# Performance work log

Hardware: AMD Instinct MI355X
Metric: run time of the kernel (lower is better)

Reference implementation:

```python
import jax, jax.numpy as jnp
import numpy as np

TEMPERATURE = 8.0  # sqrt(d_head=64)
CLAMP = 15.0
EPS = 1e-6


def setup_inputs() -> dict:
    key = jax.random.key(0)
    kq, kk, kv, km = jax.random.split(key, 4)
    B, Lq, Lk, D = 16, 2048, 2048, 64
    q = jax.random.normal(kq, (B, Lq, D), dtype=jnp.float32)
    k = jax.random.normal(kk, (B, Lk, D), dtype=jnp.float32)
    v = jax.random.normal(kv, (B, Lk, D), dtype=jnp.float32)
    mask = jax.random.randint(km, (B, Lq, Lk), 0, 2).astype(jnp.float32)
    return {"q": q, "k": k, "v": v, "mask": mask}


def masked_softmax(x, m, axis=-1):
    # clamp -> multiply by mask -> stable exp -> multiply by mask -> normalize
    x = jnp.clip(x, -CLAMP, CLAMP)
    x = x * m
    e_x = jnp.exp(x - jnp.max(x, axis=axis, keepdims=True))
    e_x = e_x * m
    return e_x / (jnp.sum(e_x, axis=axis, keepdims=True) + EPS)


def reference(q, k, v, mask):
    # scores: [B, Lq, Lk]
    attn = jnp.einsum('bqd,bkd->bqk', q, k) / TEMPERATURE
    attn = masked_softmax(attn, mask, axis=2)
    # dropout is identity in eval mode (deterministic reference)
    output = jnp.einsum('bqk,bkd->bqd', attn, v)
    return (output, attn)
```

## Files before the change

### kernel.cpp

```cpp
#include <hip/hip_runtime.h>
#include <stdint.h>

#define NB 16
#define LQ 2048
#define LK 2048
#define DH 64
#define QT 32

typedef short bf16x8 __attribute__((ext_vector_type(8)));
typedef float f32x4 __attribute__((ext_vector_type(4)));

__device__ __forceinline__ unsigned short f2bf(float f) {
    union { float f; uint32_t u; } v; v.f = f;
    uint32_t u = v.u;
    u += 0x7FFFu + ((u >> 16) & 1u);
    return (unsigned short)(u >> 16);
}
__device__ __forceinline__ float bf2f(unsigned short h) {
    union { uint32_t u; float f; } v; v.u = ((uint32_t)h) << 16;
    return v.f;
}
__device__ __forceinline__ uint32_t pack2(float lo, float hi) {
    return (uint32_t)f2bf(lo) | ((uint32_t)f2bf(hi) << 16);
}

__global__ void convert_kernel(const float* __restrict__ q, const float* __restrict__ k,
                               const float* __restrict__ v,
                               unsigned short* __restrict__ qb,
                               unsigned short* __restrict__ kb,
                               unsigned short* __restrict__ vtb) {
    int bid = blockIdx.x;
    int tid = threadIdx.x;
    if (bid < 2048) {
        const float* src = (bid < 1024) ? q : k;
        unsigned short* dst = (bid < 1024) ? qb : kb;
        int64_t off = (int64_t)(bid & 1023) * 2048 + (int64_t)tid * 8;
        float4 a = *(const float4*)(src + off);
        float4 b4 = *(const float4*)(src + off + 4);
        uint4 o;
        o.x = pack2(a.x, a.y);
        o.y = pack2(a.z, a.w);
        o.z = pack2(b4.x, b4.y);
        o.w = pack2(b4.z, b4.w);
        *(uint4*)(dst + off) = o;
    } else {
        __shared__ unsigned short tile[64][72];
        int bid2 = bid - 2048;
        int bb = bid2 >> 5, kt = bid2 & 31;
        int k0 = kt * 64;
        int krow = tid >> 2, dc = (tid & 3) * 16;
        const float* vp = v + ((int64_t)(bb * LK) + k0 + krow) * DH + dc;
        float4 x0 = *(const float4*)(vp);
        float4 x1 = *(const float4*)(vp + 4);
        float4 x2 = *(const float4*)(vp + 8);
        float4 x3 = *(const float4*)(vp + 12);
        float vals[16] = {x0.x, x0.y, x0.z, x0.w, x1.x, x1.y, x1.z, x1.w,
                          x2.x, x2.y, x2.z, x2.w, x3.x, x3.y, x3.z, x3.w};
        #pragma unroll
        for (int i = 0; i < 16; ++i) tile[dc + i][krow] = f2bf(vals[i]);
        __syncthreads();
        int d = tid >> 2, kc = (tid & 3) * 16;
        uint4 r0 = *(const uint4*)&tile[d][kc];
        uint4 r1 = *(const uint4*)&tile[d][kc + 8];
        unsigned short* op = vtb + ((int64_t)(bb * DH) + d) * LK + k0 + kc;
        *(uint4*)op = r0;
        *(uint4*)(op + 8) = r1;
    }
}

__launch_bounds__(512, 1)
__global__ void attn_kernel(const unsigned short* __restrict__ qb,
                            const unsigned short* __restrict__ kb,
                            const unsigned short* __restrict__ vtb,
                            const float* __restrict__ mask,
                            float* __restrict__ out, float* __restrict__ attn) {
    extern __shared__ char smem[];
    float* denom_part = (float*)(smem + QT * LK * 2);

    int bid = blockIdx.x;
    int swz = (bid & 7) * 128 + (bid >> 3);
    int b = swz >> 6;
    int q0 = (swz & 63) * QT;

    int tid = threadIdx.x;
    int lane = tid & 63;
    int wave = tid >> 6;
    int wm = wave >> 2, wn = wave & 3;
    int lr = lane & 15, lg = lane >> 4;

    bf16x8 qf0, qf1;
    {
        const unsigned short* qp = qb + ((int64_t)(b * LQ + q0 + wm * 16 + lr)) * DH + 8 * lg;
        qf0 = *(const bf16x8*)qp;
        qf1 = *(const bf16x8*)(qp + 32);
    }

    float dsum[4] = {0.f, 0.f, 0.f, 0.f};

    for (int kt = 0; kt < LK / 64; ++kt) {
        int kbase = kt * 64 + wn * 16;
        const unsigned short* kp = kb + ((int64_t)(b * LK + kbase + lr)) * DH + 8 * lg;
        bf16x8 kf0 = *(const bf16x8*)kp;
        bf16x8 kf1 = *(const bf16x8*)(kp + 32);
        f32x4 acc = {0.f, 0.f, 0.f, 0.f};
        acc = __builtin_amdgcn_mfma_f32_16x16x32_bf16(qf0, kf0, acc, 0, 0, 0);
        acc = __builtin_amdgcn_mfma_f32_16x16x32_bf16(qf1, kf1, acc, 0, 0, 0);
        int c = kbase + lr;
        const float* mp = mask + ((int64_t)(b * LQ + q0 + wm * 16 + lg * 4)) * LK + c;
        #pragma unroll
        for (int j = 0; j < 4; ++j) {
            int r = wm * 16 + lg * 4 + j;
            float s = acc[j] * 0.125f;
            s = fminf(fmaxf(s, -15.0f), 15.0f);
            float m = mp[(int64_t)j * LK];
            float e = __expf(s * m) * m;
            unsigned short eb = f2bf(e);
            dsum[j] += bf2f(eb);
            int byteoff = (r * 4096 + c * 2) ^ ((r & 7) << 4);
            *(unsigned short*)(smem + byteoff) = eb;
        }
    }

    #pragma unroll
    for (int j = 0; j < 4; ++j) {
        float s = dsum[j];
        s += __shfl_xor(s, 1);
        s += __shfl_xor(s, 2);
        s += __shfl_xor(s, 4);
        s += __shfl_xor(s, 8);
        if (lr == 0) denom_part[wn * 32 + wm * 16 + lg * 4 + j] = s;
    }
    __syncthreads();

    f32x4 pacc = {0.f, 0.f, 0.f, 0.f};
    {
        const unsigned short* vp = vtb + ((int64_t)(b * DH + wn * 16 + lr)) * LK + 8 * lg;
        int r = wm * 16 + lr;
        int rowoff = r * 4096;
        int sw = (r & 7) << 4;
        for (int kk = 0; kk < LK; kk += 32) {
            int byteoff = (rowoff + (kk + 8 * lg) * 2) ^ sw;
            bf16x8 ef = *(const bf16x8*)(smem + byteoff);
            bf16x8 vf = *(const bf16x8*)(vp + kk);
            pacc = __builtin_amdgcn_mfma_f32_16x16x32_bf16(ef, vf, pacc, 0, 0, 0);
        }
    }

    #pragma unroll
    for (int j = 0; j < 4; ++j) {
        int r = wm * 16 + lg * 4 + j;
        float den = denom_part[r] + denom_part[32 + r] + denom_part[64 + r] +
                    denom_part[96 + r] + 1e-6f;
        out[((int64_t)(b * LQ + q0 + r)) * DH + wn * 16 + lr] = pacc[j] / den;
    }

    {
        int r = tid >> 4;
        float den = denom_part[r] + denom_part[32 + r] + denom_part[64 + r] +
                    denom_part[96 + r] + 1e-6f;
        float inv = 1.0f / den;
        float* ap = attn + ((int64_t)(b * LQ + q0 + r)) * LK;
        int rowoff = r * 4096;
        int sw = (r & 7) << 4;
        for (int c0 = (tid & 15) * 8; c0 < LK; c0 += 128) {
            int byteoff = (rowoff + c0 * 2) ^ sw;
            bf16x8 ev = *(const bf16x8*)(smem + byteoff);
            float4 o0, o1;
            o0.x = bf2f((unsigned short)ev[0]) * inv;
            o0.y = bf2f((unsigned short)ev[1]) * inv;
            o0.z = bf2f((unsigned short)ev[2]) * inv;
            o0.w = bf2f((unsigned short)ev[3]) * inv;
            o1.x = bf2f((unsigned short)ev[4]) * inv;
            o1.y = bf2f((unsigned short)ev[5]) * inv;
            o1.z = bf2f((unsigned short)ev[6]) * inv;
            o1.w = bf2f((unsigned short)ev[7]) * inv;
            *(float4*)(ap + c0) = o0;
            *(float4*)(ap + c0 + 4) = o1;
        }
    }
}

extern "C" void kernel_launch(void* const* d_in, const int* in_sizes, int n_in,
                              void* d_out, int out_size, void* d_ws, size_t ws_size,
                              hipStream_t stream) {
    const float* q    = (const float*)d_in[0];
    const float* k    = (const float*)d_in[1];
    const float* v    = (const float*)d_in[2];
    const float* mask = (const float*)d_in[3];
    float* out  = (float*)d_out;
    float* attn = out + (int64_t)NB * LQ * DH;

    unsigned short* qb  = (unsigned short*)d_ws;
    unsigned short* kb  = qb + (int64_t)NB * LQ * DH;
    unsigned short* vtb = kb + (int64_t)NB * LK * DH;

    (void)hipFuncSetAttribute((const void*)attn_kernel,
                              hipFuncAttributeMaxDynamicSharedMemorySize, 131584);

    convert_kernel<<<2560, 256, 0, stream>>>(q, k, v, qb, kb, vtb);
    attn_kernel<<<1024, 512, 131584, stream>>>(qb, kb, vtb, mask, out, attn);
}
```

Measured before the change: 257.6 us.

## Halve query tile, prefetch K/mask next tile, split PV reduction across waves

Reduces the query tile from 32 to 16 rows so each block uses about 68KB of LDS instead of 128KB, doubling the grid and letting more blocks co-reside per CU. All 8 waves now share the same 16 query rows and split the key dimension, with software prefetch of the next K fragment and mask values to hide global latency. The PV product is split into two key halves whose partial sums are combined through shared memory before normalization. Q is reloaded per smaller tile and an extra sync is added, in exchange for better latency hiding on the mask-bound score phase.

```diff
diff --git a/kernel.cpp b/kernel.cpp
--- a/kernel.cpp
+++ b/kernel.cpp
@@ -5,7 +5,7 @@
 #define LQ 2048
 #define LK 2048
 #define DH 64
-#define QT 32
+#define QT 16
 
 typedef short bf16x8 __attribute__((ext_vector_type(8)));
 typedef float f32x4 __attribute__((ext_vector_type(4)));
@@ -68,7 +68,7 @@
     }
 }
 
-__launch_bounds__(512, 1)
+__launch_bounds__(512, 4)
 __global__ void attn_kernel(const unsigned short* __restrict__ qb,
                             const unsigned short* __restrict__ kb,
                             const unsigned short* __restrict__ vtb,
@@ -76,48 +76,70 @@
                             float* __restrict__ out, float* __restrict__ attn) {
     extern __shared__ char smem[];
     float* denom_part = (float*)(smem + QT * LK * 2);
+    float* pp         = (float*)(smem + QT * LK * 2 + 512);
 
     int bid = blockIdx.x;
-    int swz = (bid & 7) * 128 + (bid >> 3);
-    int b = swz >> 6;
-    int q0 = (swz & 63) * QT;
+    int swz = (bid & 7) * 256 + (bid >> 3);
+    int b = swz >> 7;
+    int q0 = (swz & 127) * QT;
 
     int tid = threadIdx.x;
     int lane = tid & 63;
     int wave = tid >> 6;
-    int wm = wave >> 2, wn = wave & 3;
     int lr = lane & 15, lg = lane >> 4;
 
     bf16x8 qf0, qf1;
     {
-        const unsigned short* qp = qb + ((int64_t)(b * LQ + q0 + wm * 16 + lr)) * DH + 8 * lg;
+        const unsigned short* qp = qb + ((int64_t)(b * LQ + q0 + lr)) * DH + 8 * lg;
         qf0 = *(const bf16x8*)qp;
         qf1 = *(const bf16x8*)(qp + 32);
     }
 
     float dsum[4] = {0.f, 0.f, 0.f, 0.f};
 
-    for (int kt = 0; kt < LK / 64; ++kt) {
-        int kbase = kt * 64 + wn * 16;
-        const unsigned short* kp = kb + ((int64_t)(b * LK + kbase + lr)) * DH + 8 * lg;
-        bf16x8 kf0 = *(const bf16x8*)kp;
-        bf16x8 kf1 = *(const bf16x8*)(kp + 32);
-        f32x4 acc = {0.f, 0.f, 0.f, 0.f};
-        acc = __builtin_amdgcn_mfma_f32_16x16x32_bf16(qf0, kf0, acc, 0, 0, 0);
-        acc = __builtin_amdgcn_mfma_f32_16x16x32_bf16(qf1, kf1, acc, 0, 0, 0);
-        int c = kbase + lr;
-        const float* mp = mask + ((int64_t)(b * LQ + q0 + wm * 16 + lg * 4)) * LK + c;
-        #pragma unroll
-        for (int j = 0; j < 4; ++j) {
-            int r = wm * 16 + lg * 4 + j;
-            float s = acc[j] * 0.125f;
-            s = fminf(fmaxf(s, -15.0f), 15.0f);
-            float m = mp[(int64_t)j * LK];
-            float e = __expf(s * m) * m;
-            unsigned short eb = f2bf(e);
-            dsum[j] += bf2f(eb);
-            int byteoff = (r * 4096 + c * 2) ^ ((r & 7) << 4);
-            *(unsigned short*)(smem + byteoff) = eb;
+    {
+        const int64_t krow0 = (int64_t)b * LK;
+        const float* mbase = mask + ((int64_t)(b * LQ + q0 + lg * 4)) * LK;
+        bf16x8 kf0, kf1;
+        float mr0, mr1, mr2, mr3;
+        {
+            const unsigned short* kp =
+                kb + (krow0 + wave * 16 + lr) * DH + 8 * lg;
+            kf0 = *(const bf16x8*)kp;
+            kf1 = *(const bf16x8*)(kp + 32);
+            const float* mp = mbase + wave * 16 + lr;
+            mr0 = mp[0]; mr1 = mp[LK]; mr2 = mp[2 * LK]; mr3 = mp[3 * LK];
+        }
+        for (int kt = 0; kt < LK / 128; ++kt) {
+            bf16x8 nk0, nk1;
+            float nm0, nm1, nm2, nm3;
+            if (kt < LK / 128 - 1) {
+                int nbase = (kt + 1) * 128 + wave * 16;
+                const unsigned short* kp = kb + (krow0 + nbase + lr) * DH + 8 * lg;
+                nk0 = *(const bf16x8*)kp;
+                nk1 = *(const bf16x8*)(kp + 32);
+                const float* mp = mbase + nbase + lr;
+                nm0 = mp[0]; nm1 = mp[LK]; nm2 = mp[2 * LK]; nm3 = mp[3 * LK];
+            }
+            f32x4 acc = {0.f, 0.f, 0.f, 0.f};
+            acc = __builtin_amdgcn_mfma_f32_16x16x32_bf16(qf0, kf0, acc, 0, 0, 0);
+            acc = __builtin_amdgcn_mfma_f32_16x16x32_bf16(qf1, kf1, acc, 0, 0, 0);
+            int c = kt * 128 + wave * 16 + lr;
+            float mv[4] = {mr0, mr1, mr2, mr3};
+            #pragma unroll
+            for (int j = 0; j < 4; ++j) {
+                int r = lg * 4 + j;
+                float s = acc[j] * 0.125f;
+                s = fminf(fmaxf(s, -15.0f), 15.0f);
+                float m = mv[j];
+                float e = __expf(s * m) * m;
+                unsigned short eb = f2bf(e);
+                dsum[j] += bf2f(eb);
+                int byteoff = (r * 4096 + c * 2) ^ ((r & 7) << 4);
+                *(unsigned short*)(smem + byteoff) = eb;
+            }
+            kf0 = nk0; kf1 = nk1;
+            mr0 = nm0; mr1 = nm1; mr2 = nm2; mr3 = nm3;
         }
     }
 
@@ -128,41 +150,53 @@
         s += __shfl_xor(s, 2);
         s += __shfl_xor(s, 4);
         s += __shfl_xor(s, 8);
-        if (lr == 0) denom_part[wn * 32 + wm * 16 + lg * 4 + j] = s;
+        if (lr == 0) denom_part[wave * 16 + lg * 4 + j] = s;
     }
     __syncthreads();
 
     f32x4 pacc = {0.f, 0.f, 0.f, 0.f};
-    {
-        const unsigned short* vp = vtb + ((int64_t)(b * DH + wn * 16 + lr)) * LK + 8 * lg;
-        int r = wm * 16 + lr;
-        int rowoff = r * 4096;
-        int sw = (r & 7) << 4;
-        for (int kk = 0; kk < LK; kk += 32) {
-            int byteoff = (rowoff + (kk + 8 * lg) * 2) ^ sw;
+    int cw = (wave & 3) * 16, kh = wave >> 2;
+    {
+        const unsigned short* vp =
+            vtb + ((int64_t)(b * DH + cw + lr)) * LK + kh * 1024 + 8 * lg;
+        int rowoff = lr * 4096;
+        int sw = (lr & 7) << 4;
+        int kk0 = kh * 1024;
+        for (int kk = 0; kk < 1024; kk += 32) {
+            int byteoff = (rowoff + (kk0 + kk + 8 * lg) * 2) ^ sw;
             bf16x8 ef = *(const bf16x8*)(smem + byteoff);
             bf16x8 vf = *(const bf16x8*)(vp + kk);
             pacc = __builtin_amdgcn_mfma_f32_16x16x32_bf16(ef, vf, pacc, 0, 0, 0);
         }
     }
-
-    #pragma unroll
-    for (int j = 0; j < 4; ++j) {
-        int r = wm * 16 + lg * 4 + j;
-        float den = denom_part[r] + denom_part[32 + r] + denom_part[64 + r] +
-                    denom_part[96 + r] + 1e-6f;
-        out[((int64_t)(b * LQ + q0 + r)) * DH + wn * 16 + lr] = pacc[j] / den;
-    }
-
-    {
-        int r = tid >> 4;
-        float den = denom_part[r] + denom_part[32 + r] + denom_part[64 + r] +
-                    denom_part[96 + r] + 1e-6f;
+    if (kh == 1) {
+        #pragma unroll
+        for (int j = 0; j < 4; ++j)
+            pp[(wave & 3) * 256 + (lg * 4 + j) * 16 + lr] = pacc[j];
+    }
+    __syncthreads();
+    if (kh == 0) {
+        #pragma unroll
+        for (int j = 0; j < 4; ++j) {
+            int r = lg * 4 + j;
+            float den = 1e-6f;
+            #pragma unroll
+            for (int w = 0; w < 8; ++w) den += denom_part[w * 16 + r];
+            float val = pacc[j] + pp[cw * 16 + r * 16 + lr];
+            out[((int64_t)(b * LQ + q0 + r)) * DH + cw + lr] = val / den;
+        }
+    }
+
+    {
+        int r = tid >> 5;
+        float den = 1e-6f;
+        #pragma unroll
+        for (int w = 0; w < 8; ++w) den += denom_part[w * 16 + r];
         float inv = 1.0f / den;
         float* ap = attn + ((int64_t)(b * LQ + q0 + r)) * LK;
         int rowoff = r * 4096;
         int sw = (r & 7) << 4;
-        for (int c0 = (tid & 15) * 8; c0 < LK; c0 += 128) {
+        for (int c0 = (tid & 31) * 8; c0 < LK; c0 += 256) {
             int byteoff = (rowoff + c0 * 2) ^ sw;
             bf16x8 ev = *(const bf16x8*)(smem + byteoff);
             float4 o0, o1;
@@ -195,8 +229,8 @@
     unsigned short* vtb = kb + (int64_t)NB * LK * DH;
 
     (void)hipFuncSetAttribute((const void*)attn_kernel,
-                              hipFuncAttributeMaxDynamicSharedMemorySize, 131584);
+                              hipFuncAttributeMaxDynamicSharedMemorySize, 70144);
 
     convert_kernel<<<2560, 256, 0, stream>>>(q, k, v, qb, kb, vtb);
-    attn_kernel<<<1024, 512, 131584, stream>>>(qb, kb, vtb, mask, out, attn);
-}
+    attn_kernel<<<2048, 512, 70144, stream>>>(qb, kb, vtb, mask, out, attn);
+}
```

New measurement: 236.3 us. 1.09x faster.
